# Performance work log

Hardware: AMD Instinct MI355X
Metric: run time of the kernel (lower is better)

The kernel has to match this reference:

```python
import jax, jax.numpy as jnp
import numpy as np

SR = 22050
L = 2097153            # output_size = int(SR*95.109); equals NFFT//2+1 so spectral broadcast is well-defined
NFFT = 4194304         # 2**ceil(log2(L))
BANDS = [(1.0, 4.0), (4.0, 8.0), (8.0, 13.0), (13.0, 30.0), (30.0, 100.0), (100.0, 200.0)]
SPEC = [7.83, 528.0, 396.0, 2.5, 14.1, 432.0, 6.0, 30.0]
WIN = 15               # min(15, NFFT//100)
FREQS_NP = np.fft.rfftfreq(NFFT, 1.0 / SR).astype(np.float32)
FREQS = jnp.asarray(FREQS_NP)


def _freq_mod(sig, band_w, freq_w, harm_prog, tm_w1, tm_b1, tm_w2, tm_b2, tm_w3, tm_b3):
    t = jnp.arange(L, dtype=jnp.float32)
    Xf = jnp.fft.rfft(jnp.pad(sig, (0, NFFT - L)))            # [L] complex64
    # sequential band enhancements == product of per-band multipliers
    mult = jnp.ones((L,), jnp.float32)
    for b, (lo, hi) in enumerate(BANDS):
        c = (lo + hi) / 2.0
        w = (hi - lo) / 2.0
        mask = jnp.exp(-0.5 * ((FREQS - c) / (w / 2.0)) ** 2)
        mask = jnp.where((FREQS < lo) | (FREQS > hi), 0.0, mask)
        tmod = jnp.sin(2.0 * np.pi * c * t / SR)
        mult = mult * (1.0 + mask * band_w[b] * (1.0 + 0.2 * tmod))
    # harmonic progression (identical for every specific frequency -> compute once)
    tn = (t / L)[:, None]
    h = jax.nn.relu(tn @ tm_w1 + tm_b1)
    h = jax.nn.relu(h @ tm_w2 + tm_b2)
    mp = h @ tm_w3 + tm_b3                                    # [L, 8]
    chord_idx = jnp.floor(t / L * 8.0).astype(jnp.int32) % 8
    chord = harm_prog[chord_idx] * (1.0 + mp[:, 1] * jnp.sin(2.0 * np.pi * t / L))[:, None]
    prog_mean = chord.mean()
    # specific-frequency harmonic windows (static indices; commutative multiplies)
    smult = jnp.ones((L,), jnp.float32)
    for k, f in enumerate(SPEC):
        for m in (1.0, 2.0, 3.0, 4.0, 5.0):
            hf = f * m
            if hf >= SR / 2:
                continue
            hidx = int(np.argmin(np.abs(FREQS_NP - hf)))
            s = max(0, hidx - WIN)
            e = min(L - 1, hidx + WIN)
            win = jnp.asarray(np.exp(-0.5 * ((np.arange(s, e + 1) - hidx) / (WIN / 3.0)) ** 2).astype(np.float32))
            enh = freq_w[k] * win * (1.0 / m ** 1.2) * (1.0 + prog_mean)
            smult = smult.at[s:e + 1].multiply(1.0 + enh)
    Xf = Xf * mult * smult
    mag = jnp.abs(Xf)
    ph = jnp.angle(Xf)
    mag_s = jnp.concatenate([mag[:1], mag[1:-1] * 0.7 + mag[:-2] * 0.15 + mag[2:] * 0.15, mag[-1:]])
    Xc = mag_s * jnp.exp(1j * ph)
    return jnp.fft.irfft(Xc, n=NFFT)[:L]


def _conv1d(x, w, b, stride):
    y = jax.lax.conv_general_dilated(x, w, (stride,), [(2, 2)], dimension_numbers=("NCH", "OIH", "NCH"))
    return y + b[None, :, None]


def setup_inputs() -> dict:
    key = jax.random.key(0)
    ks = jax.random.split(key, 16)
    n = lambda k, s, sc=1.0: jax.random.normal(k, s, dtype=jnp.float32) * sc
    return {
        "z": n(ks[0], (1, 1, L)),
        "condition": n(ks[1], (1, 8)),
        "band_w": jnp.full((6,), 0.5, jnp.float32),
        "freq_w": jnp.full((8,), 0.3, jnp.float32),
        "harm_prog": n(ks[2], (8, 4)),
        "tm_w1": n(ks[3], (1, 32), 0.5), "tm_b1": jnp.zeros((32,), jnp.float32),
        "tm_w2": n(ks[4], (32, 16), 0.2), "tm_b2": jnp.zeros((16,), jnp.float32),
        "tm_w3": n(ks[5], (16, 8), 0.2), "tm_b3": jnp.zeros((8,), jnp.float32),
        "c1_w": n(ks[6], (32, 1, 5), 0.3), "c1_b": jnp.zeros((32,), jnp.float32),
        "c2_w": n(ks[7], (64, 32, 5), 0.08), "c2_b": jnp.zeros((64,), jnp.float32),
        "c3_w": n(ks[8], (128, 64, 5), 0.05), "c3_b": jnp.zeros((128,), jnp.float32),
        "mx_w1": n(ks[9], (192, 256), 0.07), "mx_b1": jnp.zeros((256,), jnp.float32),
        "mx_w2": n(ks[10], (256, 1), 0.06), "mx_b2": jnp.zeros((1,), jnp.float32),
    }


def reference(z, condition, band_w, freq_w, harm_prog, tm_w1, tm_b1, tm_w2, tm_b2, tm_w3, tm_b3,
              c1_w, c1_b, c2_w, c2_b, c3_w, c3_b, mx_w1, mx_b1, mx_w2, mx_b2):
    base = _freq_mod(z[0, 0], band_w, freq_w, harm_prog, tm_w1, tm_b1, tm_w2, tm_b2, tm_w3, tm_b3)[None, None, :]
    h = jax.nn.leaky_relu(_conv1d(base, c1_w, c1_b, 2), 0.2)
    h = jax.nn.leaky_relu(_conv1d(h, c2_w, c2_b, 2), 0.2)
    h = jax.nn.leaky_relu(_conv1d(h, c3_w, c3_b, 2), 0.2)
    feat = h.mean(axis=2)                                     # [1, 128]
    emb = jnp.zeros((1, 64), jnp.float32)                     # instrument_idx=None path
    mixed = jnp.concatenate([feat, emb], axis=1)              # [1, 192]
    out = jax.nn.leaky_relu(mixed @ mx_w1 + mx_b1, 0.2) @ mx_w2 + mx_b2
    return out
```

## Files before the change

kernel.cpp:

```cpp
#include <hip/hip_runtime.h>
#include <cmath>

#define LSIG  2097153
#define MH    2097152
#define NFFTC 4194304
#define NT    262144
#define NT64  32768
#define O1C   1048577
#define O2C   524289
#define O3C   262145

#define TO3   62
#define NB3   4229

#define A_OFF    0
#define B_OFF    16777216
#define PM_OFF   58720268
#define FEAT_OFF 58720272
#define W2Q_OFF  50331664
#define W3Q_OFF  50352144
#define W1Q_OFF  50434064

struct SmultTab { int hidx[40]; float inv12[40]; int fk[40]; int maxe; };

typedef short short8 __attribute__((ext_vector_type(8)));
typedef float f32x4v __attribute__((ext_vector_type(4)));

union AFrag { uint4 q; short8 s; };
union BFrag { uint4 q; unsigned int u[4]; short8 s; };

__device__ __forceinline__ float lrelu(float a){ return a > 0.0f ? a : 0.2f*a; }

__device__ __forceinline__ float hsin(float rev){ return __builtin_amdgcn_sinf(rev); }
__device__ __forceinline__ float hcos(float rev){ return __builtin_amdgcn_cosf(rev); }

__device__ __forceinline__ unsigned int rbf(float f) {
  unsigned int u = __float_as_uint(f);
  u += 0x7fffu + ((u >> 16) & 1u);
  return u >> 16;
}
__device__ __forceinline__ unsigned int pack_bf2(float a, float b) {
  unsigned int r;
  asm("v_cvt_pk_bf16_f32 %0, %1, %2" : "=v"(r) : "v"(a), "v"(b));
  return r;
}

__device__ __forceinline__ int swz1(int pos, int dw) {
  return (pos*16 + dw) ^ (((pos >> 1) & 7) << 2);
}
__device__ __forceinline__ int swz2(int pos, int dw) {
  return (pos*32 + dw) ^ (((pos >> 1) & 7) << 2);
}

__device__ __forceinline__ float2 cadd(float2 a, float2 b){ return make_float2(a.x+b.x, a.y+b.y); }
__device__ __forceinline__ float2 csub(float2 a, float2 b){ return make_float2(a.x-b.x, a.y-b.y); }
__device__ __forceinline__ float2 cmul(float2 a, float2 b){ return make_float2(a.x*b.x - a.y*b.y, a.x*b.y + a.y*b.x); }

template<bool FWD> __device__ __forceinline__ float2 jrot(float2 z){
  return FWD ? make_float2(z.y, -z.x) : make_float2(-z.y, z.x);
}

template<bool FWD> __device__ __forceinline__ void dft8(float2 v[8]) {
  const float cq = 0.70710678118654752440f;
  const float S  = FWD ? -1.0f : 1.0f;
  float2 e0 = cadd(v[0], v[4]), e1 = csub(v[0], v[4]);
  float2 e2 = cadd(v[2], v[6]), e3 = csub(v[2], v[6]);
  float2 E0 = cadd(e0, e2), E2 = csub(e0, e2);
  float2 jt = jrot<FWD>(e3);
  float2 E1 = cadd(e1, jt), E3 = csub(e1, jt);
  float2 o0 = cadd(v[1], v[5]), o1 = csub(v[1], v[5]);
  float2 o2 = cadd(v[3], v[7]), o3 = csub(v[3], v[7]);
  float2 O0 = cadd(o0, o2), O2 = csub(o0, o2);
  float2 jo = jrot<FWD>(o3);
  float2 O1 = cadd(o1, jo), O3 = csub(o1, jo);
  float2 T1 = make_float2(cq, S*cq), T3 = make_float2(-cq, S*cq);
  float2 w1 = cmul(T1, O1);
  float2 w2 = jrot<FWD>(O2);
  float2 w3 = cmul(T3, O3);
  v[0] = cadd(E0, O0); v[4] = csub(E0, O0);
  v[1] = cadd(E1, w1); v[5] = csub(E1, w1);
  v[2] = cadd(E2, w2); v[6] = csub(E2, w2);
  v[3] = cadd(E3, w3); v[7] = csub(E3, w3);
}

template<bool FWD>
__global__ __launch_bounds__(256) void kfft8(const float2* __restrict__ src,
                                             float2* __restrict__ dst, int Ns) {
  int j = blockIdx.x*256 + threadIdx.x;
  int m = j & (Ns - 1);
  const float ssg = FWD ? -1.0f : 1.0f;
  float frac = (float)m / (float)(Ns * 8);
  float2 v[8];
  v[0] = src[j];
#pragma unroll
  for (int r = 1; r < 8; ++r) {
    float2 a = src[j + r*NT];
    float rev = frac * (float)r;
    float sn = ssg * hsin(rev), cs = hcos(rev);
    v[r] = make_float2(a.x*cs - a.y*sn, a.x*sn + a.y*cs);
  }
  dft8<FWD>(v);
  int base = ((j - m) << 3) + m;
#pragma unroll
  for (int r = 0; r < 8; ++r) dst[base + r*Ns] = v[r];
}

template<bool FWD>
__global__ __launch_bounds__(512) void kfft64(const float2* __restrict__ src,
                                              float2* __restrict__ dst, int Ns) {
  __shared__ float2 stage[4096];
  const int t = threadIdx.x;
  const int jb = blockIdx.x * 64;
  const float ssg = FWD ? -1.0f : 1.0f;
  const float invden = 1.0f / (float)(64 * Ns);
  for (int c = 0; c < 8; ++c) {
    int idx = t + 512*c;
    int jj = idx & 63, rr = idx >> 6;
    stage[jj*64 + ((rr + 9*jj) & 63)] = src[jb + jj + rr*NT64];
  }
  __syncthreads();
  const int bj = t >> 3, i = t & 7;
  const int m = (jb + bj) & (Ns - 1);
  float2 v[8];
#pragma unroll
  for (int r1 = 0; r1 < 8; ++r1) {
    float2 a = stage[bj*64 + ((8*r1 + i + 9*bj) & 63)];
    if (Ns > 1) {
      const int r = 8*r1 + i;
      float rev = (float)(m * r) * invden;
      float sn = ssg * hsin(rev), cs = hcos(rev);
      a = make_float2(a.x*cs - a.y*sn, a.x*sn + a.y*cs);
    }
    v[r1] = a;
  }
  dft8<FWD>(v);
  __syncthreads();
#pragma unroll
  for (int k1 = 0; k1 < 8; ++k1) {
    float rev = (float)(i*k1) * 0.015625f;
    float sn = ssg * hsin(rev), cs = hcos(rev);
    stage[bj*64 + ((k1*8 + i + 9*bj) & 63)] =
      make_float2(v[k1].x*cs - v[k1].y*sn, v[k1].x*sn + v[k1].y*cs);
  }
  __syncthreads();
  float2 u[8];
#pragma unroll
  for (int r0 = 0; r0 < 8; ++r0) u[r0] = stage[bj*64 + ((i*8 + r0 + 9*bj) & 63)];
  dft8<FWD>(u);
  __syncthreads();
#pragma unroll
  for (int k0 = 0; k0 < 8; ++k0)
    stage[bj*64 + ((8*k0 + i + 9*bj) & 63)] = u[k0];
  __syncthreads();
  for (int c = 0; c < 8; ++c) {
    int idx = t + 512*c;
    int jj, k;
    if (Ns == 1) { jj = idx >> 6; k = idx & 63; }
    else         { jj = idx & 63; k = idx >> 6; }
    int j2 = jb + jj, m2 = j2 & (Ns - 1);
    dst[(j2 - m2)*64 + m2 + k*Ns] = stage[jj*64 + ((k + 9*jj) & 63)];
  }
}

__global__ __launch_bounds__(512) void kfirst(
    const float* __restrict__ zin, float2* __restrict__ dst,
    const float* __restrict__ tw1, const float* __restrict__ tb1,
    const float* __restrict__ tw2, const float* __restrict__ tb2,
    const float* __restrict__ tw3, const float* __restrict__ tb3,
    const float* __restrict__ hp, float* __restrict__ pm,
    float* __restrict__ feat) {
  __shared__ float2 stage[4096];
  __shared__ float sw1[32], sb1[32], sw2[512], sb2[16], sw3[16], shp[8], sb31[1];
  __shared__ float red[512];
  const int t = threadIdx.x;
  const int bb = blockIdx.x;
  if (bb < 512) {
    const int jb = bb * 64;
    for (int c = 0; c < 8; ++c) {
      int idx = t + 512*c;
      int jj = idx & 63, rr = idx >> 6;
      int n = jb + jj + rr*NT64;
      float2 a;
      if (n < 1048576)       a = ((const float2*)zin)[n];
      else if (n == 1048576) a = make_float2(zin[2097152], 0.0f);
      else                   a = make_float2(0.0f, 0.0f);
      stage[jj*64 + ((rr + 9*jj) & 63)] = a;
    }
    __syncthreads();
    const int bj = t >> 3, i = t & 7;
    float2 v[8];
#pragma unroll
    for (int r1 = 0; r1 < 8; ++r1)
      v[r1] = stage[bj*64 + ((8*r1 + i + 9*bj) & 63)];
    dft8<true>(v);
    __syncthreads();
#pragma unroll
    for (int k1 = 0; k1 < 8; ++k1) {
      float rev = (float)(i*k1) * 0.015625f;
      float sn = -hsin(rev), cs = hcos(rev);
      stage[bj*64 + ((k1*8 + i + 9*bj) & 63)] =
        make_float2(v[k1].x*cs - v[k1].y*sn, v[k1].x*sn + v[k1].y*cs);
    }
    __syncthreads();
    float2 u[8];
#pragma unroll
    for (int r0 = 0; r0 < 8; ++r0) u[r0] = stage[bj*64 + ((i*8 + r0 + 9*bj) & 63)];
    dft8<true>(u);
    __syncthreads();
#pragma unroll
    for (int k0 = 0; k0 < 8; ++k0)
      stage[bj*64 + ((8*k0 + i + 9*bj) & 63)] = u[k0];
    __syncthreads();
    for (int c = 0; c < 8; ++c) {
      int idx = t + 512*c;
      int jj = idx >> 6, k = idx & 63;
      dst[(jb + jj)*64 + k] = stage[jj*64 + ((k + 9*jj) & 63)];
    }
    return;
  }
  if (t < 32) { sw1[t] = tw1[t]; sb1[t] = tb1[t]; }
  sw2[t] = tw2[t];
  if (t < 16) { sb2[t] = tb2[t]; sw3[t] = tw3[t*8+1]; }
  if (t < 8) { float s = 0.f; for (int j = 0; j < 4; ++j) s += hp[t*4+j]; shp[t] = s; }
  if (t == 0) sb31[0] = tb3[1];
  __syncthreads();
  const int gid = (bb - 512)*512 + t;
  if (gid < 32768) feat[gid] = 0.0f;
  const float Lf = 2097153.0f;
  float tnv[4], sv[4];
  int ci[4];
  float acc[4][16];
#pragma unroll
  for (int e = 0; e < 4; ++e) {
    float ti = (float)(gid + e*524288);
    float tn = ti / Lf;
    tnv[e] = tn;
    sv[e] = hsin(tn);
    ci[e] = ((int)floorf(tn * 8.0f)) & 7;
#pragma unroll
    for (int kk = 0; kk < 16; ++kk) acc[e][kk] = sb2[kk];
  }
  for (int j = 0; j < 32; ++j) {
    float a = sw1[j], b = sb1[j];
    float hj[4];
#pragma unroll
    for (int e = 0; e < 4; ++e) hj[e] = fmaxf(a*tnv[e] + b, 0.0f);
#pragma unroll
    for (int kk = 0; kk < 16; ++kk) {
      float w = sw2[j*16 + kk];
#pragma unroll
      for (int e = 0; e < 4; ++e) acc[e][kk] += hj[e]*w;
    }
  }
  float lsum = 0.0f;
#pragma unroll
  for (int e = 0; e < 4; ++e) {
    float mp1 = sb31[0];
#pragma unroll
    for (int kk = 0; kk < 16; ++kk) mp1 += fmaxf(acc[e][kk], 0.0f)*sw3[kk];
    lsum += shp[ci[e]] * (1.0f + mp1*sv[e]);
  }
  if (gid == 0) {
    float ti = 2097152.0f;
    float tn = ti / Lf;
    float a1[16];
    for (int kk = 0; kk < 16; ++kk) a1[kk] = sb2[kk];
    for (int j = 0; j < 32; ++j) {
      float h = fmaxf(sw1[j]*tn + sb1[j], 0.0f);
      for (int kk = 0; kk < 16; ++kk) a1[kk] += h*sw2[j*16+kk];
    }
    float mp1 = sb31[0];
    for (int kk = 0; kk < 16; ++kk) mp1 += fmaxf(a1[kk], 0.0f)*sw3[kk];
    float svx = hsin(tn);
    int cix = ((int)floorf(tn * 8.0f)) & 7;
    lsum += shp[cix] * (1.0f + mp1*svx);
  }
  red[t] = lsum;
  __syncthreads();
  for (int off = 256; off > 0; off >>= 1) {
    if (t < off) red[t] += red[t+off];
    __syncthreads();
  }
  if (t == 0) atomicAdd(pm, red[0]);
}

__device__ __forceinline__ float2 xsplit(float2 zk, float2 zm, float rev) {
  float2 s  = make_float2(zk.x + zm.x, zk.y - zm.y);
  float2 dd = make_float2(zk.x - zm.x, zk.y + zm.y);
  float sn = -hsin(rev), cs = hcos(rev);
  float2 t1 = make_float2(cs*dd.x - sn*dd.y, cs*dd.y + sn*dd.x);
  return make_float2(0.5f*(s.x + t1.y), 0.5f*(s.y - t1.x));
}
__device__ __forceinline__ float2 scale_xc(float2 c, float mg, float ms) {
  if (mg > 0.0f) { float sc = ms/mg; return make_float2(c.x*sc, c.y*sc); }
  return make_float2(ms, 0.0f);
}
__device__ __forceinline__ float2 invpack(int n, float2 a, float2 b) {
  float2 s  = make_float2(a.x + b.x, a.y - b.y);
  float2 dd = make_float2(a.x - b.x, a.y + b.y);
  float rev = (float)n * (1.0f / (float)NFFTC);
  float sn = hsin(rev), cs = hcos(rev);
  float2 xo = make_float2(0.5f*(cs*dd.x - sn*dd.y), 0.5f*(cs*dd.y + sn*dd.x));
  const float sc = 1.0f / (float)MH;
  return make_float2((0.5f*s.x - xo.y)*sc, (0.5f*s.y + xo.x)*sc);
}

__global__ __launch_bounds__(256) void kspectral(const float2* __restrict__ Z,
    float2* __restrict__ A, const float* __restrict__ bwp,
    const float* __restrict__ fwp, const float* __restrict__ pm_in, SmultTab tab,
    const float* __restrict__ c1w, const float* __restrict__ c2w,
    const float* __restrict__ c3w, unsigned short* __restrict__ w1q,
    unsigned short* __restrict__ w2q, unsigned short* __restrict__ w3q) {
  const int bb = blockIdx.x;
  const int t = threadIdx.x;
  if (bb >= 4096) {
    int i = (bb - 4096)*256 + t;
    if (i < 1024) {
      int e = i & 7, quad = (i >> 3) & 3, ch = i >> 5;
      float v = (quad == 0 && e < 5) ? c1w[ch*5 + e] : 0.0f;
      w1q[i] = (unsigned short)rbf(v);
    }
    if (i < 10240) {
      int e = i & 7, quad = (i >> 3) & 3, kt = (i >> 5) % 5, ch = i / 160;
      int c1 = quad*8 + e;
      w2q[i] = (unsigned short)rbf(c2w[ch*160 + c1*5 + kt]);
    }
    if (i < 40960) {
      int e = i & 7, quad = (i >> 3) & 3, kt = (i >> 5) % 10, ch = i / 320;
      int c2 = (kt & 1)*32 + quad*8 + e;
      w3q[i] = (unsigned short)rbf(c3w[ch*320 + c2*5 + (kt >> 1)]);
    }
    return;
  }
  __shared__ float2 Xlo[258], Xhi[258];
  __shared__ float  Mlo[258], Mhi[258];
  const int k0 = bb * 256;
  const float pm1 = 1.0f + pm_in[0] * (1.0f/8388612.0f);
  for (int w = t; w < 258; w += 256) {
    int k = k0 - 1 + w;
    float2 zk = Z[k & (MH-1)];
    float2 zm = Z[(MH - k) & (MH-1)];
    {
      float2 X = xsplit(zk, zm, (float)k * (1.0f/(float)NFFTC));
      float mv = 1.0f;
      if (k <= 38050) {
        const float blo[6] = {1.0f,4.0f,8.0f,13.0f,30.0f,100.0f};
        const float bhi[6] = {4.0f,8.0f,13.0f,30.0f,100.0f,200.0f};
        const float bcn[6] = {2.5f,6.0f,10.5f,21.5f,65.0f,150.0f};
        const float bhw[6] = {0.75f,1.0f,1.25f,4.25f,17.5f,25.0f};
        float f = (float)((double)k * (22050.0/4194304.0));
#pragma unroll
        for (int b = 0; b < 6; ++b) {
          if (f >= blo[b] && f <= bhi[b]) {
            float q = (f - bcn[b]) / bhw[b];
            float mask = expf(-0.5f*q*q);
            double frd = (double)k * ((double)bcn[b] / 22050.0);
            frd -= floor(frd);
            float tm = hsin((float)frd);
            mv *= (1.0f + mask * bwp[b] * (1.0f + 0.2f*tm));
          }
        }
      }
      if (k <= tab.maxe) {
        for (int ww = 0; ww < 40; ++ww) {
          int dlt = k - tab.hidx[ww];
          if (dlt >= -15 && dlt <= 15) {
            float x = (float)dlt * 0.2f;
            float win = expf(-0.5f*x*x);
            float enh = fwp[tab.fk[ww]] * win * tab.inv12[ww] * pm1;
            mv *= (1.0f + enh);
          }
        }
      }
      X.x *= mv; X.y *= mv;
      Xlo[w] = X; Mlo[w] = sqrtf(X.x*X.x + X.y*X.y);
    }
    {
      float2 X = xsplit(zm, zk, (float)(MH - k) * (1.0f/(float)NFFTC));
      Xhi[w] = X; Mhi[w] = sqrtf(X.x*X.x + X.y*X.y);
    }
  }
  __syncthreads();
  const int k = k0 + t, w = t + 1;
  float msl = (k == 0) ? Mlo[w] : 0.7f*Mlo[w] + 0.15f*(Mlo[w-1] + Mlo[w+1]);
  float2 xl = scale_xc(Xlo[w], Mlo[w], msl);
  float msh = (k == 0) ? Mhi[w] : 0.7f*Mhi[w] + 0.15f*(Mhi[w+1] + Mhi[w-1]);
  float2 xh = scale_xc(Xhi[w], Mhi[w], msh);
  A[k] = invpack(k, xl, xh);
  if (k >= 1) A[MH - k] = invpack(MH - k, xh, xl);
  if (bb == 4095 && t == 255) {
    float2 Xm = Xlo[257]; float Mm = Mlo[257];
    float ms = 0.7f*Mm + 0.15f*(Mlo[256] + Mhi[256]);
    float2 xm = scale_xc(Xm, Mm, ms);
    A[1048576] = invpack(1048576, xm, xm);
  }
}

__global__ __launch_bounds__(256, 4) void kconv(const float* __restrict__ x,
    const unsigned short* __restrict__ w1q, const unsigned short* __restrict__ w2q,
    const unsigned short* __restrict__ w3q, const float* __restrict__ c1b,
    const float* __restrict__ c2b, const float* __restrict__ c3b,
    float* __restrict__ feat) {
  __shared__ float sb[552];
  __shared__ unsigned int sh1[4352];
  __shared__ unsigned int sh2[4224];
  const int tid  = threadIdx.x;
  const int blk  = blockIdx.x;
  const int s3   = blk * TO3;
  const int lane = tid & 63;
  const int wv   = tid >> 6;
  const int col  = lane & 15;
  const int quad = lane >> 4;

  const uint4* W1 = (const uint4*)w1q;
  AFrag a1w[2];
#pragma unroll
  for (int mi = 0; mi < 2; ++mi)
    a1w[mi].q = W1[(mi*16 + col)*4 + quad];

  const uint4* W2 = (const uint4*)w2q;
  const int mt2 = (wv & 1) * 2;
  const int ntb2 = (wv >> 1) * 4;
  uint4 wk2[2][5];
#pragma unroll
  for (int mi = 0; mi < 2; ++mi)
#pragma unroll
    for (int kt = 0; kt < 5; ++kt)
      wk2[mi][kt] = W2[(((mt2+mi)*16 + col)*5 + kt)*4 + quad];

  float b1r[2][4], b2r[2][4];
#pragma unroll
  for (int mi = 0; mi < 2; ++mi)
#pragma unroll
    for (int r = 0; r < 4; ++r) {
      b1r[mi][r] = c1b[mi*16 + quad*4 + r];
      b2r[mi][r] = c2b[(mt2+mi)*16 + quad*4 + r];
    }

  {
    const int pb = 8*s3 - 14;
    for (int idx = tid; idx < 552; idx += 256) {
      int p = pb + idx;
      sb[idx] = (idx < 517 && p >= 0 && p < LSIG) ? x[p] : 0.0f;
    }
    if (tid < 128) sh2[4096 + tid] = 0u;
  }
  __syncthreads();

  {
    const int a1 = 4*s3 - 6;
    for (int nt = wv; nt < 17; nt += 4) {
      const int n = nt*16 + col;
      BFrag bf;
      if (quad == 0) {
        const float* ps = &sb[2*n];
        bf.u[0] = pack_bf2(ps[0], ps[1]);
        bf.u[1] = pack_bf2(ps[2], ps[3]);
        bf.u[2] = pack_bf2(ps[4], ps[5]);
        bf.u[3] = pack_bf2(ps[6], ps[7]);
      } else {
        bf.u[0] = 0u; bf.u[1] = 0u; bf.u[2] = 0u; bf.u[3] = 0u;
      }
      f32x4v acc[2];
      acc[0] = (f32x4v){b1r[0][0], b1r[0][1], b1r[0][2], b1r[0][3]};
      acc[1] = (f32x4v){b1r[1][0], b1r[1][1], b1r[1][2], b1r[1][3]};
      acc[0] = __builtin_amdgcn_mfma_f32_16x16x32_bf16(a1w[0].s, bf.s, acc[0], 0, 0, 0);
      acc[1] = __builtin_amdgcn_mfma_f32_16x16x32_bf16(a1w[1].s, bf.s, acc[1], 0, 0, 0);
      const int o1 = a1 + n;
      const bool ok = (n <= 257) && (o1 >= 0) && (o1 < O1C);
#pragma unroll
      for (int mi = 0; mi < 2; ++mi) {
        float v0 = ok ? lrelu(acc[mi][0]) : 0.0f;
        float v1 = ok ? lrelu(acc[mi][1]) : 0.0f;
        float v2 = ok ? lrelu(acc[mi][2]) : 0.0f;
        float v3 = ok ? lrelu(acc[mi][3]) : 0.0f;
        uint2 pk; pk.x = pack_bf2(v0, v1); pk.y = pack_bf2(v2, v3);
        *(uint2*)&sh1[swz1(n, mi*8 + quad*2)] = pk;
      }
    }
  }
  __syncthreads();

  f32x4v acc2[2][4];
#pragma unroll
  for (int mi = 0; mi < 2; ++mi)
#pragma unroll
    for (int nt = 0; nt < 4; ++nt)
      acc2[mi][nt] = (f32x4v){b2r[mi][0], b2r[mi][1], b2r[mi][2], b2r[mi][3]};
#pragma unroll
  for (int kt = 0; kt < 5; ++kt) {
#pragma unroll
    for (int nt = 0; nt < 4; ++nt) {
      const int n = (ntb2 + nt)*16 + col;
      const int row = 2*n + kt;
      BFrag bf;
      bf.q = *(const uint4*)&sh1[swz1(row, quad*4)];
      AFrag a0, a1; a0.q = wk2[0][kt]; a1.q = wk2[1][kt];
      acc2[0][nt] = __builtin_amdgcn_mfma_f32_16x16x32_bf16(a0.s, bf.s, acc2[0][nt], 0, 0, 0);
      acc2[1][nt] = __builtin_amdgcn_mfma_f32_16x16x32_bf16(a1.s, bf.s, acc2[1][nt], 0, 0, 0);
    }
  }

  {
    const int a2 = 2*s3 - 2;
#pragma unroll
    for (int nt = 0; nt < 4; ++nt) {
      const int p = (ntb2 + nt)*16 + col;
      const int o2 = a2 + p;
      const bool ok = (o2 >= 0) && (o2 < O2C);
#pragma unroll
      for (int mi = 0; mi < 2; ++mi) {
        float v0 = ok ? lrelu(acc2[mi][nt][0]) : 0.0f;
        float v1 = ok ? lrelu(acc2[mi][nt][1]) : 0.0f;
        float v2 = ok ? lrelu(acc2[mi][nt][2]) : 0.0f;
        float v3 = ok ? lrelu(acc2[mi][nt][3]) : 0.0f;
        const int dwb = (mt2+mi)*8 + quad*2;
        uint2 pk; pk.x = pack_bf2(v0, v1); pk.y = pack_bf2(v2, v3);
        *(uint2*)&sh2[swz2(p, dwb)] = pk;
      }
    }
  }
  __syncthreads();

  {
    const uint4* W3 = (const uint4*)w3q;
    const int slot = (blk & 255) * 128;
#pragma unroll
    for (int pass = 0; pass < 2; ++pass) {
      const int mt = wv + 4*pass;
      uint4 wk3[10];
#pragma unroll
      for (int kt = 0; kt < 10; ++kt)
        wk3[kt] = W3[((mt*16 + col)*10 + kt)*4 + quad];
      float b3r[4];
#pragma unroll
      for (int r = 0; r < 4; ++r) b3r[r] = c3b[mt*16 + quad*4 + r];
      f32x4v acc3[4];
#pragma unroll
      for (int nt = 0; nt < 4; ++nt)
        acc3[nt] = (f32x4v){b3r[0], b3r[1], b3r[2], b3r[3]};
#pragma unroll
      for (int kt = 0; kt < 10; ++kt) {
        const int tap = kt >> 1;
        const int hh  = (kt & 1) * 16;
#pragma unroll
        for (int nt = 0; nt < 4; ++nt) {
          const int n = nt*16 + col;
          const int row = 2*n + tap;
          BFrag bf;
          bf.q = *(const uint4*)&sh2[swz2(row, hh + quad*4)];
          AFrag a; a.q = wk3[kt];
          acc3[nt] = __builtin_amdgcn_mfma_f32_16x16x32_bf16(a.s, bf.s, acc3[nt], 0, 0, 0);
        }
      }
#pragma unroll
      for (int r = 0; r < 4; ++r) {
        const int ch = mt*16 + quad*4 + r;
        float v = 0.0f;
#pragma unroll
        for (int nt = 0; nt < 4; ++nt) {
          const int n = nt*16 + col;
          const bool ok = (n < TO3) && (s3 + n < O3C);
          if (ok) v += lrelu(acc3[nt][r]);
        }
        v += __shfl_xor(v, 1);
        v += __shfl_xor(v, 2);
        v += __shfl_xor(v, 4);
        v += __shfl_xor(v, 8);
        if (col == 0) atomicAdd(&feat[slot + ch], v);
      }
    }
  }
}

__global__ __launch_bounds__(256) void kfinal(const float* __restrict__ feat,
    const float* __restrict__ mw1, const float* __restrict__ mb1,
    const float* __restrict__ mw2, const float* __restrict__ mb2,
    float* __restrict__ out) {
  __shared__ float sfeat[128];
  __shared__ float red[256];
  const int tid = threadIdx.x;
  if (tid < 128) {
    float s = 0.0f;
    for (int sl = 0; sl < 256; ++sl) s += feat[sl*128 + tid];
    sfeat[tid] = s / 262145.0f;
  }
  __syncthreads();
  float y = mb1[tid];
  for (int i = 0; i < 128; ++i) y += sfeat[i] * mw1[i*256 + tid];
  y = y > 0.0f ? y : 0.2f*y;
  red[tid] = y * mw2[tid];
  __syncthreads();
  for (int off = 128; off > 0; off >>= 1) {
    if (tid < off) red[tid] += red[tid+off];
    __syncthreads();
  }
  if (tid == 0) out[0] = red[0] + mb2[0];
}

extern "C" void kernel_launch(void* const* d_in, const int* in_sizes, int n_in,
                              void* d_out, int out_size, void* d_ws, size_t ws_size,
                              hipStream_t stream) {
  (void)in_sizes; (void)n_in; (void)out_size; (void)ws_size;
  const float* z   = (const float*)d_in[0];
  const float* bw  = (const float*)d_in[2];
  const float* fw  = (const float*)d_in[3];
  const float* hp  = (const float*)d_in[4];
  const float* tw1 = (const float*)d_in[5];
  const float* tb1 = (const float*)d_in[6];
  const float* tw2 = (const float*)d_in[7];
  const float* tb2 = (const float*)d_in[8];
  const float* tw3 = (const float*)d_in[9];
  const float* tb3 = (const float*)d_in[10];
  const float* c1w = (const float*)d_in[11];
  const float* c1b = (const float*)d_in[12];
  const float* c2w = (const float*)d_in[13];
  const float* c2b = (const float*)d_in[14];
  const float* c3w = (const float*)d_in[15];
  const float* c3b = (const float*)d_in[16];
  const float* mw1 = (const float*)d_in[17];
  const float* mb1 = (const float*)d_in[18];
  const float* mw2 = (const float*)d_in[19];
  const float* mb2 = (const float*)d_in[20];

  char* wsb = (char*)d_ws;
  float2* A    = (float2*)(wsb + A_OFF);
  float2* B    = (float2*)(wsb + B_OFF);
  float*  PM   = (float*)(wsb + PM_OFF);
  float*  FEAT = (float*)(wsb + FEAT_OFF);
  unsigned short* W1Q = (unsigned short*)(wsb + W1Q_OFF);
  unsigned short* W2Q = (unsigned short*)(wsb + W2Q_OFF);
  unsigned short* W3Q = (unsigned short*)(wsb + W3Q_OFF);

  SmultTab tab;
  {
    const double spec[8] = {7.83, 528.0, 396.0, 2.5, 14.1, 432.0, 6.0, 30.0};
    int n = 0, maxe = 0;
    for (int kk = 0; kk < 8; ++kk)
      for (int m = 1; m <= 5; ++m) {
        double hf = spec[kk] * (double)m;
        if (hf >= 11025.0) continue;
        int hidx = (int)std::floor(hf * (4194304.0/22050.0) + 0.5);
        tab.hidx[n]  = hidx;
        tab.inv12[n] = (float)(1.0/std::pow((double)m, 1.2));
        tab.fk[n]    = kk;
        if (hidx + 15 > maxe) maxe = hidx + 15;
        ++n;
      }
    tab.maxe = maxe;
  }

  (void)hipMemsetAsync(wsb + PM_OFF, 0, 4, stream);

  kfirst<<<1536,512,0,stream>>>(z, A, tw1,tb1,tw2,tb2,tw3,tb3,hp, PM, FEAT);

  kfft64<true ><<<512,512,0,stream>>>(A, B, 64);
  kfft64<true ><<<512,512,0,stream>>>(B, A, 4096);
  kfft8 <true ><<<1024,256,0,stream>>>(A, B, 262144);

  kspectral<<<4256,256,0,stream>>>(B, A, bw, fw, PM, tab, c1w, c2w, c3w, W1Q, W2Q, W3Q);

  kfft64<false><<<512,512,0,stream>>>(A, B, 1);
  kfft64<false><<<512,512,0,stream>>>(B, A, 64);
  kfft64<false><<<512,512,0,stream>>>(A, B, 4096);
  kfft8 <false><<<1024,256,0,stream>>>(B, A, 262144);

  kconv<<<NB3,256,0,stream>>>((const float*)A, W1Q, W2Q, W3Q, c1b, c2b, c3b, FEAT);
  kfinal<<<1,256,0,stream>>>(FEAT, mw1, mb1, mw2, mb2, (float*)d_out);
}
```

Measured before the change: 285.6 us.

## Restructure FFT as three radix-128 passes instead of radix-64/radix-8 stages

Replaces the 64-64-64-8 Stockham decomposition of the 2^21-point complex FFT with three radix-128 passes, each done in shared memory as a 16x8 split. This removes one global read/write pass from both the forward and inverse transforms. The last inverse pass also skips writing the upper half of the output that the convolution never reads. In exchange, more twiddle work runs per pass, and only half the threads are active in the second sub-stage, which may lower utilisation.

```diff
diff --git a/kernel.cpp b/kernel.cpp
--- a/kernel.cpp
+++ b/kernel.cpp
@@ -4,8 +4,7 @@
 #define LSIG  2097153
 #define MH    2097152
 #define NFFTC 4194304
-#define NT    262144
-#define NT64  32768
+#define NT128 16384
 #define O1C   1048577
 #define O2C   524289
 #define O3C   262145
@@ -54,7 +53,6 @@
 
 __device__ __forceinline__ float2 cadd(float2 a, float2 b){ return make_float2(a.x+b.x, a.y+b.y); }
 __device__ __forceinline__ float2 csub(float2 a, float2 b){ return make_float2(a.x-b.x, a.y-b.y); }
-__device__ __forceinline__ float2 cmul(float2 a, float2 b){ return make_float2(a.x*b.x - a.y*b.y, a.x*b.y + a.y*b.x); }
 
 template<bool FWD> __device__ __forceinline__ float2 jrot(float2 z){
   return FWD ? make_float2(z.y, -z.x) : make_float2(-z.y, z.x);
@@ -73,10 +71,9 @@
   float2 O0 = cadd(o0, o2), O2 = csub(o0, o2);
   float2 jo = jrot<FWD>(o3);
   float2 O1 = cadd(o1, jo), O3 = csub(o1, jo);
-  float2 T1 = make_float2(cq, S*cq), T3 = make_float2(-cq, S*cq);
-  float2 w1 = cmul(T1, O1);
+  float2 w1 = make_float2(cq*O1.x - S*cq*O1.y, cq*O1.y + S*cq*O1.x);
   float2 w2 = jrot<FWD>(O2);
-  float2 w3 = cmul(T3, O3);
+  float2 w3 = make_float2(-cq*O3.x - S*cq*O3.y, -cq*O3.y + S*cq*O3.x);
   v[0] = cadd(E0, O0); v[4] = csub(E0, O0);
   v[1] = cadd(E1, w1); v[5] = csub(E1, w1);
   v[2] = cadd(E2, w2); v[6] = csub(E2, w2);
@@ -84,81 +81,83 @@
 }
 
 template<bool FWD>
-__global__ __launch_bounds__(256) void kfft8(const float2* __restrict__ src,
-                                             float2* __restrict__ dst, int Ns) {
-  int j = blockIdx.x*256 + threadIdx.x;
-  int m = j & (Ns - 1);
+__device__ __forceinline__ void fft128_body(float2* stage, int t, int jb, int Ns) {
   const float ssg = FWD ? -1.0f : 1.0f;
-  float frac = (float)m / (float)(Ns * 8);
-  float2 v[8];
-  v[0] = src[j];
-#pragma unroll
-  for (int r = 1; r < 8; ++r) {
-    float2 a = src[j + r*NT];
-    float rev = frac * (float)r;
-    float sn = ssg * hsin(rev), cs = hcos(rev);
-    v[r] = make_float2(a.x*cs - a.y*sn, a.x*sn + a.y*cs);
-  }
-  dft8<FWD>(v);
-  int base = ((j - m) << 3) + m;
-#pragma unroll
-  for (int r = 0; r < 8; ++r) dst[base + r*Ns] = v[r];
-}
-
-template<bool FWD>
-__global__ __launch_bounds__(512) void kfft64(const float2* __restrict__ src,
-                                              float2* __restrict__ dst, int Ns) {
+  const float invden = 1.0f / (float)(128 * Ns);
+  {
+    const int jj = t >> 4, b = t & 15;
+    const int m = (jb + jj) & (Ns - 1);
+    float2 v[8];
+#pragma unroll
+    for (int a = 0; a < 8; ++a) {
+      const int r = 16*a + b;
+      float2 x = stage[jj*128 + ((r + 9*jj) & 127)];
+      if (Ns > 1) {
+        float rev = (float)(m * r) * invden;
+        float sn = ssg * hsin(rev), cs = hcos(rev);
+        x = make_float2(x.x*cs - x.y*sn, x.x*sn + x.y*cs);
+      }
+      v[a] = x;
+    }
+    dft8<FWD>(v);
+#pragma unroll
+    for (int d = 0; d < 8; ++d)
+      stage[jj*128 + ((16*d + b + 9*jj) & 127)] = v[d];
+  }
+  __syncthreads();
+  {
+    float2 y[16];
+    const int jj = (t & 255) >> 3, d = t & 7;
+    if (t < 256) {
+#pragma unroll
+      for (int b = 0; b < 16; ++b) {
+        float2 x = stage[jj*128 + ((16*d + b + 9*jj) & 127)];
+        float rev = (float)(b*d) * 0.0078125f;
+        float sn = ssg * hsin(rev), cs = hcos(rev);
+        y[b] = make_float2(x.x*cs - x.y*sn, x.x*sn + x.y*cs);
+      }
+    }
+    __syncthreads();
+    if (t < 256) {
+      float2 E[8], O[8];
+#pragma unroll
+      for (int b = 0; b < 8; ++b) { E[b] = y[2*b]; O[b] = y[2*b+1]; }
+      dft8<FWD>(E);
+      dft8<FWD>(O);
+#pragma unroll
+      for (int c = 0; c < 8; ++c) {
+        float rev = (float)c * 0.0625f;
+        float sn = ssg * hsin(rev), cs = hcos(rev);
+        float2 To = make_float2(O[c].x*cs - O[c].y*sn, O[c].x*sn + O[c].y*cs);
+        stage[jj*128 + ((8*c + d + 9*jj) & 127)]      = cadd(E[c], To);
+        stage[jj*128 + ((8*c + 64 + d + 9*jj) & 127)] = csub(E[c], To);
+      }
+    }
+  }
+  __syncthreads();
+}
+
+template<bool FWD, bool TRUNC>
+__global__ __launch_bounds__(512) void kfft128(const float2* __restrict__ src,
+                                               float2* __restrict__ dst, int Ns) {
   __shared__ float2 stage[4096];
   const int t = threadIdx.x;
-  const int jb = blockIdx.x * 64;
-  const float ssg = FWD ? -1.0f : 1.0f;
-  const float invden = 1.0f / (float)(64 * Ns);
+  const int jb = blockIdx.x * 32;
   for (int c = 0; c < 8; ++c) {
     int idx = t + 512*c;
-    int jj = idx & 63, rr = idx >> 6;
-    stage[jj*64 + ((rr + 9*jj) & 63)] = src[jb + jj + rr*NT64];
-  }
-  __syncthreads();
-  const int bj = t >> 3, i = t & 7;
-  const int m = (jb + bj) & (Ns - 1);
-  float2 v[8];
-#pragma unroll
-  for (int r1 = 0; r1 < 8; ++r1) {
-    float2 a = stage[bj*64 + ((8*r1 + i + 9*bj) & 63)];
-    if (Ns > 1) {
-      const int r = 8*r1 + i;
-      float rev = (float)(m * r) * invden;
-      float sn = ssg * hsin(rev), cs = hcos(rev);
-      a = make_float2(a.x*cs - a.y*sn, a.x*sn + a.y*cs);
-    }
-    v[r1] = a;
-  }
-  dft8<FWD>(v);
-  __syncthreads();
-#pragma unroll
-  for (int k1 = 0; k1 < 8; ++k1) {
-    float rev = (float)(i*k1) * 0.015625f;
-    float sn = ssg * hsin(rev), cs = hcos(rev);
-    stage[bj*64 + ((k1*8 + i + 9*bj) & 63)] =
-      make_float2(v[k1].x*cs - v[k1].y*sn, v[k1].x*sn + v[k1].y*cs);
-  }
-  __syncthreads();
-  float2 u[8];
-#pragma unroll
-  for (int r0 = 0; r0 < 8; ++r0) u[r0] = stage[bj*64 + ((i*8 + r0 + 9*bj) & 63)];
-  dft8<FWD>(u);
-  __syncthreads();
-#pragma unroll
-  for (int k0 = 0; k0 < 8; ++k0)
-    stage[bj*64 + ((8*k0 + i + 9*bj) & 63)] = u[k0];
-  __syncthreads();
+    int jj = idx & 31, rr = idx >> 5;
+    stage[jj*128 + ((rr + 9*jj) & 127)] = src[jb + jj + rr*NT128];
+  }
+  __syncthreads();
+  fft128_body<FWD>(stage, t, jb, Ns);
   for (int c = 0; c < 8; ++c) {
     int idx = t + 512*c;
     int jj, k;
-    if (Ns == 1) { jj = idx >> 6; k = idx & 63; }
-    else         { jj = idx & 63; k = idx >> 6; }
+    if (Ns == 1) { jj = idx >> 7; k = idx & 127; }
+    else         { jj = idx & 31; k = idx >> 5; }
     int j2 = jb + jj, m2 = j2 & (Ns - 1);
-    dst[(j2 - m2)*64 + m2 + k*Ns] = stage[jj*64 + ((k + 9*jj) & 63)];
+    if (TRUNC && !(k < 64 || (k == 64 && j2 == 0))) continue;
+    dst[(j2 - m2)*128 + m2 + k*Ns] = stage[jj*128 + ((k + 9*jj) & 127)];
   }
 }
 
@@ -175,46 +174,23 @@
   const int t = threadIdx.x;
   const int bb = blockIdx.x;
   if (bb < 512) {
-    const int jb = bb * 64;
+    const int jb = bb * 32;
     for (int c = 0; c < 8; ++c) {
       int idx = t + 512*c;
-      int jj = idx & 63, rr = idx >> 6;
-      int n = jb + jj + rr*NT64;
+      int jj = idx & 31, rr = idx >> 5;
+      int n = jb + jj + rr*NT128;
       float2 a;
       if (n < 1048576)       a = ((const float2*)zin)[n];
       else if (n == 1048576) a = make_float2(zin[2097152], 0.0f);
       else                   a = make_float2(0.0f, 0.0f);
-      stage[jj*64 + ((rr + 9*jj) & 63)] = a;
+      stage[jj*128 + ((rr + 9*jj) & 127)] = a;
     }
     __syncthreads();
-    const int bj = t >> 3, i = t & 7;
-    float2 v[8];
-#pragma unroll
-    for (int r1 = 0; r1 < 8; ++r1)
-      v[r1] = stage[bj*64 + ((8*r1 + i + 9*bj) & 63)];
-    dft8<true>(v);
-    __syncthreads();
-#pragma unroll
-    for (int k1 = 0; k1 < 8; ++k1) {
-      float rev = (float)(i*k1) * 0.015625f;
-      float sn = -hsin(rev), cs = hcos(rev);
-      stage[bj*64 + ((k1*8 + i + 9*bj) & 63)] =
-        make_float2(v[k1].x*cs - v[k1].y*sn, v[k1].x*sn + v[k1].y*cs);
-    }
-    __syncthreads();
-    float2 u[8];
-#pragma unroll
-    for (int r0 = 0; r0 < 8; ++r0) u[r0] = stage[bj*64 + ((i*8 + r0 + 9*bj) & 63)];
-    dft8<true>(u);
-    __syncthreads();
-#pragma unroll
-    for (int k0 = 0; k0 < 8; ++k0)
-      stage[bj*64 + ((8*k0 + i + 9*bj) & 63)] = u[k0];
-    __syncthreads();
+    fft128_body<true>(stage, t, jb, 1);
     for (int c = 0; c < 8; ++c) {
       int idx = t + 512*c;
-      int jj = idx >> 6, k = idx & 63;
-      dst[(jb + jj)*64 + k] = stage[jj*64 + ((k + 9*jj) & 63)];
+      int jj = idx >> 7, k = idx & 127;
+      dst[(jb + jj)*128 + k] = stage[jj*128 + ((k + 9*jj) & 127)];
     }
     return;
   }
@@ -654,16 +630,14 @@
 
   kfirst<<<1536,512,0,stream>>>(z, A, tw1,tb1,tw2,tb2,tw3,tb3,hp, PM, FEAT);
 
-  kfft64<true ><<<512,512,0,stream>>>(A, B, 64);
-  kfft64<true ><<<512,512,0,stream>>>(B, A, 4096);
-  kfft8 <true ><<<1024,256,0,stream>>>(A, B, 262144);
-
-  kspectral<<<4256,256,0,stream>>>(B, A, bw, fw, PM, tab, c1w, c2w, c3w, W1Q, W2Q, W3Q);
-
-  kfft64<false><<<512,512,0,stream>>>(A, B, 1);
-  kfft64<false><<<512,512,0,stream>>>(B, A, 64);
-  kfft64<false><<<512,512,0,stream>>>(A, B, 4096);
-  kfft8 <false><<<1024,256,0,stream>>>(B, A, 262144);
+  kfft128<true,false><<<512,512,0,stream>>>(A, B, 128);
+  kfft128<true,false><<<512,512,0,stream>>>(B, A, 16384);
+
+  kspectral<<<4256,256,0,stream>>>(A, B, bw, fw, PM, tab, c1w, c2w, c3w, W1Q, W2Q, W3Q);
+
+  kfft128<false,false><<<512,512,0,stream>>>(B, A, 1);
+  kfft128<false,false><<<512,512,0,stream>>>(A, B, 128);
+  kfft128<false,true ><<<512,512,0,stream>>>(B, A, 16384);
 
   kconv<<<NB3,256,0,stream>>>((const float*)A, W1Q, W2Q, W3Q, c1b, c2b, c3b, FEAT);
   kfinal<<<1,256,0,stream>>>(FEAT, mw1, mb1, mw2, mb2, (float*)d_out);
```

After: 278.8 us. -2.4%, faster.
